# Kernel optimization log

Hardware: AMD Instinct MI355X
Metric: run time of the kernel (lower is better)

The kernel has to match this reference:

```python
import jax, jax.numpy as jnp
import numpy as np

B, S, DM, H = 2, 2048, 512, 8
DH = DM // H


def setup_inputs() -> dict:
    key = jax.random.key(0)
    ks = jax.random.split(key, 20)
    sc = 0.02
    d = {}
    d["q"] = jax.random.normal(ks[0], (B, S, DM), jnp.float32)
    d["k"] = jax.random.normal(ks[1], (B, S, DM), jnp.float32)
    d["v"] = jax.random.normal(ks[2], (B, S, DM), jnp.float32)
    d["xdiff"] = jax.random.normal(ks[3], (B, S, S), jnp.float32)
    d["mask"] = jax.random.randint(ks[4], (B, 1, 1, S), 0, 2, jnp.int32)
    # learned params (keras Dense: kernel + bias)
    d["Wq"] = jax.random.normal(ks[5], (DM, DM), jnp.float32) * sc
    d["bq"] = jnp.zeros((DM,), jnp.float32)
    d["Wk"] = jax.random.normal(ks[6], (DM, DM), jnp.float32) * sc
    d["bk"] = jnp.zeros((DM,), jnp.float32)
    d["Wv"] = jax.random.normal(ks[7], (DM, DM), jnp.float32) * sc
    d["bv"] = jnp.zeros((DM,), jnp.float32)
    d["Wa"] = jax.random.normal(ks[8], (DM, H), jnp.float32) * sc
    d["ba"] = jnp.zeros((H,), jnp.float32)
    d["Wb"] = jax.random.normal(ks[9], (DM, H), jnp.float32) * sc
    d["bb"] = jnp.zeros((H,), jnp.float32)
    d["Wo"] = jax.random.normal(ks[10], (DM, DM), jnp.float32) * sc
    d["bo"] = jnp.zeros((DM,), jnp.float32)
    return d


def reference(q, k, v, xdiff, mask, Wq, bq, Wk, bk, Wv, bv, Wa, ba, Wb, bb, Wo, bo):
    b, s, dm = q.shape
    h, dh = H, DH
    qp = q @ Wq + bq            # [B,S,DM]
    kp = k @ Wk + bk
    vp = v @ Wv + bv
    # per-head alpha/beta from projected q: [B,S,H] -> [B,H,S]
    a = jnp.transpose(qp @ Wa + ba, (0, 2, 1))
    bb_ = jnp.transpose(qp @ Wb + bb, (0, 2, 1))
    # split heads -> [B,H,S,DH]
    qh = qp.reshape(b, s, h, dh).transpose(0, 2, 1, 3)
    kh = kp.reshape(b, s, h, dh).transpose(0, 2, 1, 3)
    vh = vp.reshape(b, s, h, dh).transpose(0, 2, 1, 3)
    logits = jnp.einsum('bhqd,bhkd->bhqk', qh, kh) / jnp.sqrt(jnp.float32(dh))
    logits = logits + mask.astype(jnp.float32) * (-1e9)
    xd = xdiff[:, None]          # [B,1,S,S] broadcast over heads
    logits = logits + a[..., None] * xd + bb_[..., None] * (xd * xd)
    attn = jax.nn.softmax(logits, axis=-1)
    out = jnp.einsum('bhqk,bhkd->bhqd', attn, vh)
    out = out.transpose(0, 2, 1, 3).reshape(b, s, dm)
    return out @ Wo + bo, attn
```

## Files before the change

kernel.cpp:

```cpp
#include <hip/hip_runtime.h>
#include <stdint.h>

#define BB 2
#define SS 2048
#define DMODEL 512
#define NH 8
#define DHD 64

typedef __attribute__((ext_vector_type(8))) short bf16x8;
typedef __attribute__((ext_vector_type(4))) short s16x4;
typedef __attribute__((ext_vector_type(4))) float fx4;

__device__ __forceinline__ short f2bf(float f) {
    union { float f; uint32_t u; } c; c.f = f;
    uint32_t u = c.u;
    u += 0x7fffu + ((u >> 16) & 1u);
    return (short)(u >> 16);
}
__device__ __forceinline__ float bf2f(short s) {
    union { uint32_t u; float f; } c; c.u = ((uint32_t)(uint16_t)s) << 16;
    return c.f;
}

__global__ __launch_bounds__(256, 4) void qkv_gemm_k(
    const float* __restrict__ q, const float* __restrict__ k, const float* __restrict__ v,
    const float* __restrict__ Wq, const float* __restrict__ bq,
    const float* __restrict__ Wk, const float* __restrict__ bk,
    const float* __restrict__ Wv, const float* __restrict__ bv,
    short* __restrict__ qp, short* __restrict__ kp, short* __restrict__ vT)
{
    __shared__ short As[64 * 40];
    __shared__ short Bs[64 * 40];
    const int z = blockIdx.z;
    const float* Af   = (z == 0) ? q  : (z == 1) ? k  : v;
    const float* W    = (z == 0) ? Wq : (z == 1) ? Wk : Wv;
    const float* bias = (z == 0) ? bq : (z == 1) ? bk : bv;
    short* Cp         = (z == 0) ? qp : (z == 1) ? kp : vT;

    const int tid = threadIdx.x;
    const int w = tid >> 6, lane = tid & 63;
    const int cl = lane & 15, quad = lane >> 4;
    const int mi = w >> 1, ni = w & 1;
    const int m0 = blockIdx.x * 64, n0 = blockIdx.y * 64;
    fx4 acc[2][2] = {};

    for (int k0 = 0; k0 < DMODEL; k0 += 32) {
#pragma unroll
        for (int it = 0; it < 2; ++it) {
            int idx = tid + it * 256;
            int row = idx >> 3, kq = (idx & 7) * 4;
            const float4 vv = *(const float4*)&Af[(size_t)(m0 + row) * DMODEL + k0 + kq];
            s16x4 sv;
            sv.x = f2bf(vv.x); sv.y = f2bf(vv.y); sv.z = f2bf(vv.z); sv.w = f2bf(vv.w);
            *(s16x4*)&As[row * 40 + kq] = sv;
        }
#pragma unroll
        for (int it = 0; it < 2; ++it) {
            int idx = tid + it * 256;
            int kk = idx >> 4, nq = (idx & 15) * 4;
            const float4 vv = *(const float4*)&W[(size_t)(k0 + kk) * DMODEL + n0 + nq];
            Bs[(nq + 0) * 40 + kk] = f2bf(vv.x);
            Bs[(nq + 1) * 40 + kk] = f2bf(vv.y);
            Bs[(nq + 2) * 40 + kk] = f2bf(vv.z);
            Bs[(nq + 3) * 40 + kk] = f2bf(vv.w);
        }
        __syncthreads();
        bf16x8 af[2], bfr[2];
#pragma unroll
        for (int i = 0; i < 2; ++i)
            af[i] = *(const bf16x8*)&As[(mi * 32 + i * 16 + cl) * 40 + quad * 8];
#pragma unroll
        for (int j = 0; j < 2; ++j)
            bfr[j] = *(const bf16x8*)&Bs[(ni * 32 + j * 16 + cl) * 40 + quad * 8];
#pragma unroll
        for (int i = 0; i < 2; ++i)
#pragma unroll
            for (int j = 0; j < 2; ++j)
                acc[i][j] = __builtin_amdgcn_mfma_f32_16x16x32_bf16(af[i], bfr[j], acc[i][j], 0, 0, 0);
        __syncthreads();
    }
#pragma unroll
    for (int i = 0; i < 2; ++i) {
#pragma unroll
        for (int j = 0; j < 2; ++j) {
            int col = n0 + ni * 32 + j * 16 + cl;
            float bv = bias[col];
            if (z == 2) {
                int row0 = m0 + mi * 32 + i * 16 + quad * 4;
                int bb_ = row0 >> 11, sr = row0 & (SS - 1);
                s16x4 o;
                o.x = f2bf(acc[i][j][0] + bv);
                o.y = f2bf(acc[i][j][1] + bv);
                o.z = f2bf(acc[i][j][2] + bv);
                o.w = f2bf(acc[i][j][3] + bv);
                *(s16x4*)&Cp[((size_t)(bb_ * DMODEL + col)) * SS + sr] = o;
            } else {
#pragma unroll
                for (int r = 0; r < 4; ++r) {
                    int row = m0 + mi * 32 + i * 16 + quad * 4 + r;
                    Cp[(size_t)row * DMODEL + col] = f2bf(acc[i][j][r] + bv);
                }
            }
        }
    }
}

__global__ __launch_bounds__(256, 4) void out_gemm_k(
    const short* __restrict__ Ab, const float* __restrict__ W,
    const float* __restrict__ bias, float* __restrict__ Cp)
{
    __shared__ short As[64 * 40];
    __shared__ short Bs[64 * 40];
    const int tid = threadIdx.x;
    const int w = tid >> 6, lane = tid & 63;
    const int cl = lane & 15, quad = lane >> 4;
    const int mi = w >> 1, ni = w & 1;
    const int m0 = blockIdx.x * 64, n0 = blockIdx.y * 64;
    fx4 acc[2][2] = {};

    for (int k0 = 0; k0 < DMODEL; k0 += 32) {
#pragma unroll
        for (int it = 0; it < 2; ++it) {
            int idx = tid + it * 256;
            int row = idx >> 3, kq = (idx & 7) * 4;
            *(s16x4*)&As[row * 40 + kq] =
                *(const s16x4*)&Ab[(size_t)(m0 + row) * DMODEL + k0 + kq];
        }
#pragma unroll
        for (int it = 0; it < 2; ++it) {
            int idx = tid + it * 256;
            int kk = idx >> 4, nq = (idx & 15) * 4;
            const float4 vv = *(const float4*)&W[(size_t)(k0 + kk) * DMODEL + n0 + nq];
            Bs[(nq + 0) * 40 + kk] = f2bf(vv.x);
            Bs[(nq + 1) * 40 + kk] = f2bf(vv.y);
            Bs[(nq + 2) * 40 + kk] = f2bf(vv.z);
            Bs[(nq + 3) * 40 + kk] = f2bf(vv.w);
        }
        __syncthreads();
        bf16x8 af[2], bfr[2];
#pragma unroll
        for (int i = 0; i < 2; ++i)
            af[i] = *(const bf16x8*)&As[(mi * 32 + i * 16 + cl) * 40 + quad * 8];
#pragma unroll
        for (int j = 0; j < 2; ++j)
            bfr[j] = *(const bf16x8*)&Bs[(ni * 32 + j * 16 + cl) * 40 + quad * 8];
#pragma unroll
        for (int i = 0; i < 2; ++i)
#pragma unroll
            for (int j = 0; j < 2; ++j)
                acc[i][j] = __builtin_amdgcn_mfma_f32_16x16x32_bf16(af[i], bfr[j], acc[i][j], 0, 0, 0);
        __syncthreads();
    }
#pragma unroll
    for (int i = 0; i < 2; ++i)
#pragma unroll
        for (int j = 0; j < 2; ++j) {
            int col = n0 + ni * 32 + j * 16 + cl;
            float bv = bias[col];
#pragma unroll
            for (int r = 0; r < 4; ++r) {
                int row = m0 + mi * 32 + i * 16 + quad * 4 + r;
                Cp[(size_t)row * DMODEL + col] = acc[i][j][r] + bv;
            }
        }
}

__global__ __launch_bounds__(64) void ab_k(
    const short* __restrict__ qp,
    const float* __restrict__ Wa, const float* __restrict__ ba,
    const float* __restrict__ Wb, const float* __restrict__ bbias,
    float* __restrict__ a_ws, float* __restrict__ b_ws)
{
    const int r = blockIdx.x;
    const int b = r >> 11, s = r & 2047;
    const int lane = threadIdx.x;
    float qv[8];
    s16x4 q0 = *(const s16x4*)&qp[(size_t)r * DMODEL + lane * 8];
    s16x4 q1 = *(const s16x4*)&qp[(size_t)r * DMODEL + lane * 8 + 4];
    qv[0] = bf2f(q0.x); qv[1] = bf2f(q0.y); qv[2] = bf2f(q0.z); qv[3] = bf2f(q0.w);
    qv[4] = bf2f(q1.x); qv[5] = bf2f(q1.y); qv[6] = bf2f(q1.z); qv[7] = bf2f(q1.w);
    float pa[8] = {}, pb[8] = {};
#pragma unroll
    for (int kk = 0; kk < 8; ++kk) {
        int k = lane * 8 + kk;
        const float4 wa0 = *(const float4*)&Wa[k * 8];
        const float4 wa1 = *(const float4*)&Wa[k * 8 + 4];
        const float4 wb0 = *(const float4*)&Wb[k * 8];
        const float4 wb1 = *(const float4*)&Wb[k * 8 + 4];
        float qk = qv[kk];
        pa[0] += qk * wa0.x; pa[1] += qk * wa0.y; pa[2] += qk * wa0.z; pa[3] += qk * wa0.w;
        pa[4] += qk * wa1.x; pa[5] += qk * wa1.y; pa[6] += qk * wa1.z; pa[7] += qk * wa1.w;
        pb[0] += qk * wb0.x; pb[1] += qk * wb0.y; pb[2] += qk * wb0.z; pb[3] += qk * wb0.w;
        pb[4] += qk * wb1.x; pb[5] += qk * wb1.y; pb[6] += qk * wb1.z; pb[7] += qk * wb1.w;
    }
#pragma unroll
    for (int h = 0; h < 8; ++h) {
#pragma unroll
        for (int off = 1; off < 64; off <<= 1) {
            pa[h] += __shfl_xor(pa[h], off);
            pb[h] += __shfl_xor(pb[h], off);
        }
    }
    if (lane == 0) {
#pragma unroll
        for (int h = 0; h < 8; ++h) {
            a_ws[(b * NH + h) * SS + s] = pa[h] + ba[h];
            b_ws[(b * NH + h) * SS + s] = pb[h] + bbias[h];
        }
    }
}

__global__ __launch_bounds__(512, 2) void attn_k(
    const short* __restrict__ qp, const short* __restrict__ kp, const short* __restrict__ vT,
    const float* __restrict__ a_ws, const float* __restrict__ b_ws,
    const float* __restrict__ xdiff, const int* __restrict__ mask,
    float* __restrict__ attn, short* __restrict__ ao)
{
    __shared__ char smem[32768];
    __shared__ float redm[128], reds[128];

    const int tid = threadIdx.x;
    const int w = tid >> 6, lane = tid & 63;
    const int cl = lane & 15, quad = lane >> 4;

    const int wg = blockIdx.x;
    const int sp = wg >> 3, xcd = wg & 7;
    const int h = sp & 7;
    const int bqt = xcd * 32 + (sp >> 3);
    const int b = bqt >> 7, qt = bqt & 127;
    const int q0 = qt * 16;
    const int bS = b * SS;

    const float LOG2E = 1.44269504f;

    bf16x8 qf[2];
#pragma unroll
    for (int kc = 0; kc < 2; ++kc)
        qf[kc] = *(const bf16x8*)&qp[(size_t)(bS + q0 + cl) * DMODEL + h * DHD + kc * 32 + quad * 8];

    float ra[4], rb[4];
#pragma unroll
    for (int r = 0; r < 4; ++r) {
        int qi = q0 + quad * 4 + r;
        ra[r] = a_ws[(b * NH + h) * SS + qi] * LOG2E;
        rb[r] = b_ws[(b * NH + h) * SS + qi] * LOG2E;
    }

    const int j0w = w * 256;
    fx4 s[4][4];
    float rmax[4] = {-3e38f, -3e38f, -3e38f, -3e38f};

#pragma unroll
    for (int t = 0; t < 4; ++t) {
        const int j0 = j0w + t * 64;
        fx4 qk[4] = {};
        __builtin_amdgcn_s_setprio(1);
#pragma unroll
        for (int nb = 0; nb < 4; ++nb)
#pragma unroll
            for (int kc = 0; kc < 2; ++kc) {
                bf16x8 kf = *(const bf16x8*)&kp[(size_t)(bS + j0 + nb * 16 + cl) * DMODEL + h * DHD + kc * 32 + quad * 8];
                qk[nb] = __builtin_amdgcn_mfma_f32_16x16x32_bf16(qf[kc], kf, qk[nb], 0, 0, 0);
            }
        __builtin_amdgcn_s_setprio(0);
#pragma unroll
        for (int nb = 0; nb < 4; ++nb) {
            const int j = j0 + nb * 16 + cl;
            const float mv = -1.442695e9f * (float)mask[bS + j];
#pragma unroll
            for (int r = 0; r < 4; ++r) {
                const int qi = q0 + quad * 4 + r;
                const float xd = xdiff[(size_t)(bS + qi) * SS + j];
                float v = qk[nb][r] * 0.18033688f + mv + ra[r] * xd + rb[r] * (xd * xd);
                s[t][nb][r] = v;
                rmax[r] = fmaxf(rmax[r], v);
            }
        }
    }

#pragma unroll
    for (int off = 1; off < 16; off <<= 1)
#pragma unroll
        for (int r = 0; r < 4; ++r)
            rmax[r] = fmaxf(rmax[r], __shfl_xor(rmax[r], off));
    if (cl == 0)
#pragma unroll
        for (int r = 0; r < 4; ++r) redm[w * 16 + quad * 4 + r] = rmax[r];
    __syncthreads();
    float gm[4];
#pragma unroll
    for (int r = 0; r < 4; ++r) {
        int i = quad * 4 + r;
        float m0_ = fmaxf(redm[i],      redm[16 + i]);
        float m1_ = fmaxf(redm[32 + i], redm[48 + i]);
        float m2_ = fmaxf(redm[64 + i], redm[80 + i]);
        float m3_ = fmaxf(redm[96 + i], redm[112 + i]);
        gm[r] = fmaxf(fmaxf(m0_, m1_), fmaxf(m2_, m3_));
    }

    float rsum[4] = {};
#pragma unroll
    for (int t = 0; t < 4; ++t)
#pragma unroll
        for (int nb = 0; nb < 4; ++nb)
#pragma unroll
            for (int r = 0; r < 4; ++r) {
                float e = exp2f(s[t][nb][r] - gm[r]);
                s[t][nb][r] = e;
                rsum[r] += e;
            }
#pragma unroll
    for (int off = 1; off < 16; off <<= 1)
#pragma unroll
        for (int r = 0; r < 4; ++r)
            rsum[r] += __shfl_xor(rsum[r], off);
    if (cl == 0)
#pragma unroll
        for (int r = 0; r < 4; ++r) reds[w * 16 + quad * 4 + r] = rsum[r];
    __syncthreads();
    float gs[4];
#pragma unroll
    for (int r = 0; r < 4; ++r) {
        int i = quad * 4 + r;
        float t0 = reds[i]      + reds[16 + i] + reds[32 + i] + reds[48 + i];
        float t1 = reds[64 + i] + reds[80 + i] + reds[96 + i] + reds[112 + i];
        gs[r] = 1.0f / (t0 + t1);
    }

    fx4 oacc[4] = {};
    float* attn_bh = attn + (size_t)(b * NH + h) * SS * SS;
    short* psw = (short*)smem + w * (16 * 72);
    const size_t vbase = (size_t)((b * NH + h) * DHD) * SS;
#pragma unroll
    for (int t = 0; t < 4; ++t) {
        const int j0 = j0w + t * 64;
#pragma unroll
        for (int nb = 0; nb < 4; ++nb) {
            const int j = j0 + nb * 16 + cl;
#pragma unroll
            for (int r = 0; r < 4; ++r) {
                float p = s[t][nb][r] * gs[r];
                __builtin_nontemporal_store(p, &attn_bh[(size_t)(q0 + quad * 4 + r) * SS + j]);
                psw[(quad * 4 + r) * 72 + nb * 16 + cl] = f2bf(p);
            }
        }
        bf16x8 pf[2];
#pragma unroll
        for (int kc = 0; kc < 2; ++kc)
            pf[kc] = *(const bf16x8*)&psw[cl * 72 + kc * 32 + quad * 8];
        __builtin_amdgcn_s_setprio(1);
#pragma unroll
        for (int nb = 0; nb < 4; ++nb)
#pragma unroll
            for (int kc = 0; kc < 2; ++kc) {
                bf16x8 vf = *(const bf16x8*)&vT[vbase + (size_t)(nb * 16 + cl) * SS + j0 + kc * 32 + quad * 8];
                oacc[nb] = __builtin_amdgcn_mfma_f32_16x16x32_bf16(pf[kc], vf, oacc[nb], 0, 0, 0);
            }
        __builtin_amdgcn_s_setprio(0);
    }

    __syncthreads();
    float* ored = (float*)smem;
#pragma unroll
    for (int nb = 0; nb < 4; ++nb)
#pragma unroll
        for (int r = 0; r < 4; ++r)
            ored[w * 1024 + (quad * 4 + r) * 64 + nb * 16 + cl] = oacc[nb][r];
    __syncthreads();
    if (tid < 256) {
        int i = tid >> 4, dq = (tid & 15) * 4;
        float sx = 0, sy = 0, sz = 0, sw = 0;
#pragma unroll
        for (int ww = 0; ww < 8; ++ww) {
            const float4 vv = *(const float4*)&ored[ww * 1024 + i * 64 + dq];
            sx += vv.x; sy += vv.y; sz += vv.z; sw += vv.w;
        }
        s16x4 o;
        o.x = f2bf(sx); o.y = f2bf(sy); o.z = f2bf(sz); o.w = f2bf(sw);
        *(s16x4*)&ao[(size_t)(bS + q0 + i) * DMODEL + h * DHD + dq] = o;
    }
}

extern "C" void kernel_launch(void* const* d_in, const int* in_sizes, int n_in,
                              void* d_out, int out_size, void* d_ws, size_t ws_size,
                              hipStream_t stream)
{
    (void)in_sizes; (void)n_in; (void)out_size; (void)ws_size;
    const float* q     = (const float*)d_in[0];
    const float* k     = (const float*)d_in[1];
    const float* v     = (const float*)d_in[2];
    const float* xdiff = (const float*)d_in[3];
    const int*   mask  = (const int*)d_in[4];
    const float* Wq = (const float*)d_in[5];
    const float* bq = (const float*)d_in[6];
    const float* Wk = (const float*)d_in[7];
    const float* bk = (const float*)d_in[8];
    const float* Wv = (const float*)d_in[9];
    const float* bv = (const float*)d_in[10];
    const float* Wa = (const float*)d_in[11];
    const float* ba = (const float*)d_in[12];
    const float* Wb = (const float*)d_in[13];
    const float* bb = (const float*)d_in[14];
    const float* Wo = (const float*)d_in[15];
    const float* bo = (const float*)d_in[16];

    char* ws = (char*)d_ws;
    short* qp   = (short*)(ws + 0);
    short* kp   = (short*)(ws + 4194304);
    short* vT   = (short*)(ws + 8388608);
    float* a_ws = (float*)(ws + 12582912);
    float* b_ws = (float*)(ws + 12713984);
    short* ao   = (short*)(ws + 12845056);

    float* out  = (float*)d_out;
    float* attn = out + (size_t)BB * SS * DMODEL;

    hipLaunchKernelGGL(qkv_gemm_k, dim3(64, 8, 3), dim3(256), 0, stream,
                       q, k, v, Wq, bq, Wk, bk, Wv, bv, qp, kp, vT);
    hipLaunchKernelGGL(ab_k, dim3(4096), dim3(64), 0, stream, qp, Wa, ba, Wb, bb, a_ws, b_ws);
    hipLaunchKernelGGL(attn_k, dim3(2048), dim3(512), 0, stream,
                       qp, kp, vT, a_ws, b_ws, xdiff, mask, attn, ao);
    hipLaunchKernelGGL(out_gemm_k, dim3(64, 8), dim3(256), 0, stream, ao, Wo, bo, out);
}
```

Baseline: 538.8 us.

## Fold Wa/Wb into Wq and compute alpha/beta inside the QKV GEMM launch

Precomputes Wq@Wa and Wq@Wb (plus the folded biases) in a small kernel, so alpha/beta come straight from the raw q input. The work runs as an extra z-slice of the QKV GEMM grid, which removes the separate ab_k launch and its dependency on qp. The attention kernel's launch bounds also change from 2 to 1 block per SM, which lets it use more registers but lowers occupancy. The weight-fold kernel is serial over 512 per thread and adds one more launch.

```diff
diff --git a/kernel.cpp b/kernel.cpp
--- a/kernel.cpp
+++ b/kernel.cpp
@@ -22,23 +22,93 @@
     return c.f;
 }
 
+__global__ __launch_bounds__(256) void wab_fuse_k(
+    const float* __restrict__ Wq, const float* __restrict__ bq,
+    const float* __restrict__ Wa, const float* __restrict__ ba,
+    const float* __restrict__ Wb, const float* __restrict__ bbias,
+    float* __restrict__ Wqa, float* __restrict__ cab)
+{
+    const int idx = blockIdx.x * 256 + threadIdx.x;
+    const int d = idx >> 4, h = idx & 15;
+    const float* Wab = (h < 8) ? Wa : Wb;
+    const int hh = h & 7;
+    float acc = 0.f;
+    for (int n = 0; n < DMODEL; ++n)
+        acc += Wq[(size_t)d * DMODEL + n] * Wab[n * 8 + hh];
+    Wqa[d * 16 + h] = acc;
+    if (blockIdx.x == 0 && threadIdx.x < 16) {
+        const int h2 = threadIdx.x;
+        const float* Wab2 = (h2 < 8) ? Wa : Wb;
+        const float* bias2 = (h2 < 8) ? ba : bbias;
+        const int hh2 = h2 & 7;
+        float c = 0.f;
+        for (int n = 0; n < DMODEL; ++n)
+            c += bq[n] * Wab2[n * 8 + hh2];
+        cab[h2] = c + bias2[hh2];
+    }
+}
+
 __global__ __launch_bounds__(256, 4) void qkv_gemm_k(
     const float* __restrict__ q, const float* __restrict__ k, const float* __restrict__ v,
     const float* __restrict__ Wq, const float* __restrict__ bq,
     const float* __restrict__ Wk, const float* __restrict__ bk,
     const float* __restrict__ Wv, const float* __restrict__ bv,
-    short* __restrict__ qp, short* __restrict__ kp, short* __restrict__ vT)
+    const float* __restrict__ Wqa, const float* __restrict__ cab,
+    short* __restrict__ qp, short* __restrict__ kp, short* __restrict__ vT,
+    float* __restrict__ a_ws, float* __restrict__ b_ws)
 {
-    __shared__ short As[64 * 40];
-    __shared__ short Bs[64 * 40];
+    __shared__ char smem_raw[512 * 17 * 4];
+    const int tid = threadIdx.x;
+    const int w = tid >> 6, lane = tid & 63;
     const int z = blockIdx.z;
+
+    if (z == 3) {
+        float* WqaS = (float*)smem_raw;
+        for (int i = tid; i < 8192; i += 256) {
+            int kr = i >> 4, h = i & 15;
+            WqaS[kr * 17 + h] = Wqa[i];
+        }
+        __syncthreads();
+        const int lin = blockIdx.x * 8 + blockIdx.y;
+#pragma unroll
+        for (int rr = 0; rr < 2; ++rr) {
+            const int r = lin * 8 + w * 2 + rr;
+            const int b = r >> 11, srow = r & (SS - 1);
+            float qv[8];
+#pragma unroll
+            for (int kk = 0; kk < 8; ++kk)
+                qv[kk] = q[(size_t)r * DMODEL + kk * 64 + lane];
+            float acc[16] = {};
+#pragma unroll
+            for (int kk = 0; kk < 8; ++kk) {
+                const float* wrow = &WqaS[(kk * 64 + lane) * 17];
+#pragma unroll
+                for (int h = 0; h < 16; ++h)
+                    acc[h] += qv[kk] * wrow[h];
+            }
+#pragma unroll
+            for (int h = 0; h < 16; ++h)
+#pragma unroll
+                for (int off = 1; off < 64; off <<= 1)
+                    acc[h] += __shfl_xor(acc[h], off);
+            if (lane == 0) {
+#pragma unroll
+                for (int h = 0; h < 8; ++h) {
+                    a_ws[(b * NH + h) * SS + srow] = acc[h] + cab[h];
+                    b_ws[(b * NH + h) * SS + srow] = acc[8 + h] + cab[8 + h];
+                }
+            }
+        }
+        return;
+    }
+
+    short* As = (short*)smem_raw;
+    short* Bs = (short*)(smem_raw + 64 * 40 * 2);
     const float* Af   = (z == 0) ? q  : (z == 1) ? k  : v;
     const float* W    = (z == 0) ? Wq : (z == 1) ? Wk : Wv;
     const float* bias = (z == 0) ? bq : (z == 1) ? bk : bv;
     short* Cp         = (z == 0) ? qp : (z == 1) ? kp : vT;
 
-    const int tid = threadIdx.x;
-    const int w = tid >> 6, lane = tid & 63;
     const int cl = lane & 15, quad = lane >> 4;
     const int mi = w >> 1, ni = w & 1;
     const int m0 = blockIdx.x * 64, n0 = blockIdx.y * 64;
@@ -165,52 +235,7 @@
         }
 }
 
-__global__ __launch_bounds__(64) void ab_k(
-    const short* __restrict__ qp,
-    const float* __restrict__ Wa, const float* __restrict__ ba,
-    const float* __restrict__ Wb, const float* __restrict__ bbias,
-    float* __restrict__ a_ws, float* __restrict__ b_ws)
-{
-    const int r = blockIdx.x;
-    const int b = r >> 11, s = r & 2047;
-    const int lane = threadIdx.x;
-    float qv[8];
-    s16x4 q0 = *(const s16x4*)&qp[(size_t)r * DMODEL + lane * 8];
-    s16x4 q1 = *(const s16x4*)&qp[(size_t)r * DMODEL + lane * 8 + 4];
-    qv[0] = bf2f(q0.x); qv[1] = bf2f(q0.y); qv[2] = bf2f(q0.z); qv[3] = bf2f(q0.w);
-    qv[4] = bf2f(q1.x); qv[5] = bf2f(q1.y); qv[6] = bf2f(q1.z); qv[7] = bf2f(q1.w);
-    float pa[8] = {}, pb[8] = {};
-#pragma unroll
-    for (int kk = 0; kk < 8; ++kk) {
-        int k = lane * 8 + kk;
-        const float4 wa0 = *(const float4*)&Wa[k * 8];
-        const float4 wa1 = *(const float4*)&Wa[k * 8 + 4];
-        const float4 wb0 = *(const float4*)&Wb[k * 8];
-        const float4 wb1 = *(const float4*)&Wb[k * 8 + 4];
-        float qk = qv[kk];
-        pa[0] += qk * wa0.x; pa[1] += qk * wa0.y; pa[2] += qk * wa0.z; pa[3] += qk * wa0.w;
-        pa[4] += qk * wa1.x; pa[5] += qk * wa1.y; pa[6] += qk * wa1.z; pa[7] += qk * wa1.w;
-        pb[0] += qk * wb0.x; pb[1] += qk * wb0.y; pb[2] += qk * wb0.z; pb[3] += qk * wb0.w;
-        pb[4] += qk * wb1.x; pb[5] += qk * wb1.y; pb[6] += qk * wb1.z; pb[7] += qk * wb1.w;
-    }
-#pragma unroll
-    for (int h = 0; h < 8; ++h) {
-#pragma unroll
-        for (int off = 1; off < 64; off <<= 1) {
-            pa[h] += __shfl_xor(pa[h], off);
-            pb[h] += __shfl_xor(pb[h], off);
-        }
-    }
-    if (lane == 0) {
-#pragma unroll
-        for (int h = 0; h < 8; ++h) {
-            a_ws[(b * NH + h) * SS + s] = pa[h] + ba[h];
-            b_ws[(b * NH + h) * SS + s] = pb[h] + bbias[h];
-        }
-    }
-}
-
-__global__ __launch_bounds__(512, 2) void attn_k(
+__global__ __launch_bounds__(512, 1) void attn_k(
     const short* __restrict__ qp, const short* __restrict__ kp, const short* __restrict__ vT,
     const float* __restrict__ a_ws, const float* __restrict__ b_ws,
     const float* __restrict__ xdiff, const int* __restrict__ mask,
@@ -411,13 +436,16 @@
     float* a_ws = (float*)(ws + 12582912);
     float* b_ws = (float*)(ws + 12713984);
     short* ao   = (short*)(ws + 12845056);
+    float* Wqa  = (float*)(ws + 17039360);
+    float* cab  = (float*)(ws + 17072128);
 
     float* out  = (float*)d_out;
     float* attn = out + (size_t)BB * SS * DMODEL;
 
-    hipLaunchKernelGGL(qkv_gemm_k, dim3(64, 8, 3), dim3(256), 0, stream,
-                       q, k, v, Wq, bq, Wk, bk, Wv, bv, qp, kp, vT);
-    hipLaunchKernelGGL(ab_k, dim3(4096), dim3(64), 0, stream, qp, Wa, ba, Wb, bb, a_ws, b_ws);
+    hipLaunchKernelGGL(wab_fuse_k, dim3(32), dim3(256), 0, stream,
+                       Wq, bq, Wa, ba, Wb, bb, Wqa, cab);
+    hipLaunchKernelGGL(qkv_gemm_k, dim3(64, 8, 4), dim3(256), 0, stream,
+                       q, k, v, Wq, bq, Wk, bk, Wv, bv, Wqa, cab, qp, kp, vT, a_ws, b_ws);
     hipLaunchKernelGGL(attn_k, dim3(2048), dim3(512), 0, stream,
                        qp, kp, vT, a_ws, b_ws, xdiff, mask, attn, ao);
     hipLaunchKernelGGL(out_gemm_k, dim3(64, 8), dim3(256), 0, stream, ao, Wo, bo, out);
```

After: 558.4 us. +3.6%, slower.
